# Kernel tuning notes

Measured on AMD Instinct MI355X. Metric: run time of the kernel, lower is better.

The kernel has to match this reference:

```python
import jax, jax.numpy as jnp
import numpy as np

N = 50000      # nodes
E = 800000     # edges
DIN, DH, DE, DOUT = 3, 32 and 3 or 3, 32, 1
DIN, DH, DE, DOUT = 3, 256, 32, 1
L = 5          # residual blocks
NEG_SLOPE = 0.2
EPS = 1e-16


def setup_inputs() -> dict:
    key = jax.random.key(0)
    ks = jax.random.split(key, 18)
    s = lambda d: 1.0 / np.sqrt(d)
    inp = {
        'x': jax.random.normal(ks[0], (N, DIN), jnp.float32),
        'edge_index': jax.random.randint(ks[1], (2, E), 0, N, jnp.int64),
        'edge_attr': jax.random.normal(ks[2], (E, DE), jnp.float32),
        # lin0 / lin1
        'W0': jax.random.normal(ks[3], (DIN, DH), jnp.float32) * s(DIN),
        'b0': jnp.zeros((DH,), jnp.float32),
        'W1': jax.random.normal(ks[4], (DH, DOUT), jnp.float32) * s(DH),
        'b1': jnp.zeros((DOUT,), jnp.float32),
        # per-block GAT params (stacked over L)
        'Wg': jax.random.normal(ks[5], (L, DH, DH), jnp.float32) * s(DH),
        'bg': jnp.zeros((L, DH), jnp.float32),
        'a_src': jax.random.normal(ks[6], (L, DH), jnp.float32) * s(DH),
        'a_dst': jax.random.normal(ks[7], (L, DH), jnp.float32) * s(DH),
        'We': jax.random.normal(ks[8], (L, DE, DH), jnp.float32) * s(DE),
        'a_e': jax.random.normal(ks[9], (L, DH), jnp.float32) * s(DH),
        # per-block mean-conv params
        'Ws': jax.random.normal(ks[10], (L, DH, DH), jnp.float32) * s(DH),
        'Wn': jax.random.normal(ks[11], (L, DH, DH), jnp.float32) * s(DH),
        'bm': jnp.zeros((L, DH), jnp.float32),
    }
    return inp


def _segment_softmax(logits, seg, n):
    m = jax.ops.segment_max(logits, seg, num_segments=n)          # [N]
    ex = jnp.exp(logits - m[seg])                                  # [E]
    den = jax.ops.segment_sum(ex, seg, num_segments=n)            # [N]
    return ex / (den[seg] + EPS)


def _block(x, src, dst, edge_attr, deg, Wg, bg, a_src, a_dst, We, a_e, Ws, Wn, bm):
    # GAT attention message passing (single head, edge-feature-aware logits)
    h = x @ Wg                                                     # [N,DH]
    logit = ((h * a_src).sum(-1)[src]
             + (h * a_dst).sum(-1)[dst]
             + ((edge_attr @ We) * a_e).sum(-1))                   # [E]
    logit = jax.nn.leaky_relu(logit, NEG_SLOPE)
    alpha = _segment_softmax(logit, dst, x.shape[0])               # [E]
    agg = jax.ops.segment_sum(alpha[:, None] * h[src], dst, num_segments=x.shape[0])
    h1 = jax.nn.relu(agg + bg)                                     # [N,DH]
    # mean-aggregation graph conv
    mean_nbr = jax.ops.segment_sum(h1[src], dst, num_segments=x.shape[0]) / deg[:, None]
    h2 = jax.nn.relu(h1 @ Ws + mean_nbr @ Wn + bm)
    return h2 + x                                                  # residual


def reference(x, edge_index, edge_attr, W0, b0, W1, b1, Wg, bg, a_src, a_dst, We, a_e, Ws, Wn, bm):
    src, dst = edge_index[0], edge_index[1]
    n = x.shape[0]
    deg = jnp.maximum(jax.ops.segment_sum(jnp.ones((src.shape[0],), x.dtype), dst, num_segments=n), 1.0)
    h = x @ W0 + b0
    for i in range(L):
        h = _block(h, src, dst, edge_attr, deg,
                   Wg[i], bg[i], a_src[i], a_dst[i], We[i], a_e[i], Ws[i], Wn[i], bm[i])
    return h @ W1 + b1
```

## Files before the change

kernel.cpp:

```cpp
#include <hip/hip_runtime.h>
#include <hip/hip_bf16.h>

#define DH 256
#define DE 32
#define NLAYERS 5
#define NEG_SLOPE 0.2f
#define EPSV 1e-16f
#define SEG 512

typedef __attribute__((ext_vector_type(8))) short bf16x8;
typedef __attribute__((ext_vector_type(4))) float f32x4;

__device__ inline float bf2f(unsigned short u) {
    unsigned x = ((unsigned)u) << 16;
    union { unsigned u; float f; } c; c.u = x; return c.f;
}
__device__ inline unsigned short f2bf(float f) {
    union { float f; unsigned u; } c; c.f = f;
    unsigned b = c.u;
    unsigned r = (b + 0x7FFF + ((b >> 16) & 1)) >> 16;
    return (unsigned short)r;
}

__global__ void k_count(const int* __restrict__ dst, int* __restrict__ cnt, int E) {
    int e = blockIdx.x * 256 + threadIdx.x;
    if (e < E) atomicAdd(&cnt[dst[e]], 1);
}

__global__ void k_part(const int* __restrict__ cnt, int* __restrict__ part, int n) {
    int b = blockIdx.x, t = threadIdx.x;
    int i = b * SEG + t;
    int v = (i < n) ? cnt[i] : 0;
    for (int d = 32; d; d >>= 1) v += __shfl_down(v, d);
    __shared__ int ws[8];
    int lane = t & 63, w = t >> 6;
    if (lane == 0) ws[w] = v;
    __syncthreads();
    if (t == 0) {
        int s = 0;
        #pragma unroll
        for (int k = 0; k < 8; ++k) s += ws[k];
        part[b] = s;
    }
}

__global__ void k_scanp(const int* __restrict__ part, int* __restrict__ base,
                        int* __restrict__ off, int nblk, int n, int total) {
    int t = threadIdx.x;
    int lane = t & 63, w = t >> 6;
    __shared__ int wsum[2];
    int v = (t < nblk) ? part[t] : 0;
    int incl = v;
    for (int d = 1; d < 64; d <<= 1) {
        int u = __shfl_up(incl, d);
        if (lane >= d) incl += u;
    }
    if (lane == 63) wsum[w] = incl;
    __syncthreads();
    int add = (w == 1) ? wsum[0] : 0;
    if (t < nblk) base[t] = incl - v + add;
    if (t == 0) off[n] = total;
}

__global__ void k_emit(const int* __restrict__ cnt, const int* __restrict__ base,
                       int* __restrict__ off, float* __restrict__ invd, int n) {
    int b = blockIdx.x, t = threadIdx.x;
    int i = b * SEG + t;
    int c = (i < n) ? cnt[i] : 0;
    int lane = t & 63, w = t >> 6;
    int incl = c;
    for (int d = 1; d < 64; d <<= 1) {
        int u = __shfl_up(incl, d);
        if (lane >= d) incl += u;
    }
    __shared__ int ws[8];
    if (lane == 63) ws[w] = incl;
    __syncthreads();
    int add = 0;
    for (int k = 0; k < w; ++k) add += ws[k];
    if (i < n) {
        off[i] = base[b] + add + incl - c;
        invd[i] = 1.0f / (float)max(c, 1);
    }
}

__global__ void k_fill(const int* __restrict__ src, const int* __restrict__ dst,
                       const int* __restrict__ off, int* __restrict__ cur,
                       int* __restrict__ csrc, int* __restrict__ pos, int E) {
    int e = blockIdx.x * 256 + threadIdx.x;
    if (e >= E) return;
    int d = dst[e];
    int p = off[d] + atomicAdd(&cur[d], 1);
    csrc[p] = src[e];
    pos[e] = p;
}

__global__ void k_we_ae(const float* __restrict__ We, const float* __restrict__ a_e,
                        float* __restrict__ out) {
    int t = threadIdx.x;
    if (t >= NLAYERS * DE) return;
    int l = t >> 5, d = t & 31;
    const float* w = We + ((size_t)l * DE + d) * DH;
    const float* ae = a_e + (size_t)l * DH;
    float s = 0.f;
    for (int j = 0; j < DH; ++j) s += w[j] * ae[j];
    out[t] = s;
}

__global__ void k_elogit(const float* __restrict__ ea, const float* __restrict__ we_ae,
                         const int* __restrict__ pos, float* __restrict__ elogp, int E) {
    __shared__ float w[NLAYERS * DE];
    if (threadIdx.x < NLAYERS * DE) w[threadIdx.x] = we_ae[threadIdx.x];
    __syncthreads();
    int e = blockIdx.x * 256 + threadIdx.x;
    if (e >= E) return;
    const float4* p = (const float4*)(ea + (size_t)e * DE);
    float r[NLAYERS] = {0, 0, 0, 0, 0};
    #pragma unroll
    for (int i = 0; i < DE / 4; ++i) {
        float4 x = p[i];
        #pragma unroll
        for (int l = 0; l < NLAYERS; ++l) {
            r[l] += x.x * w[l * DE + i * 4 + 0] + x.y * w[l * DE + i * 4 + 1] +
                    x.z * w[l * DE + i * 4 + 2] + x.w * w[l * DE + i * 4 + 3];
        }
    }
    int q = pos[e];
    #pragma unroll
    for (int l = 0; l < NLAYERS; ++l) elogp[(size_t)l * E + q] = r[l];
}

__global__ void k_wt(const float* __restrict__ Wg, const float* __restrict__ Ws,
                     const float* __restrict__ Wn, unsigned short* __restrict__ Wt) {
    __shared__ float tile[32][33];
    int z = blockIdx.z;
    const float* W = z < 5 ? Wg + (size_t)z * DH * DH
                   : (z < 10 ? Ws + (size_t)(z - 5) * DH * DH
                             : Wn + (size_t)(z - 10) * DH * DH);
    unsigned short* out = Wt + (size_t)z * DH * DH;
    int c0 = blockIdx.x * 32, r0 = blockIdx.y * 32;
    int tx = threadIdx.x, ty = threadIdx.y;
    for (int j = ty; j < 32; j += 8) tile[j][tx] = W[(size_t)(r0 + j) * DH + c0 + tx];
    __syncthreads();
    for (int j = ty; j < 32; j += 8)
        out[(size_t)(c0 + j) * DH + r0 + tx] = f2bf(tile[tx][j]);
}

__global__ void k_lin0(const float* __restrict__ x, const float* __restrict__ W0,
                       const float* __restrict__ b0, unsigned short* __restrict__ hb, int n) {
    int node = blockIdx.x;
    int c = threadIdx.x;
    if (node >= n) return;
    float x0 = x[(size_t)node * 3 + 0];
    float x1 = x[(size_t)node * 3 + 1];
    float x2 = x[(size_t)node * 3 + 2];
    float v = b0[c] + x0 * W0[c] + x1 * W0[DH + c] + x2 * W0[2 * DH + c];
    hb[(size_t)node * DH + c] = f2bf(v);
}

__global__ void k_dots(const unsigned short* __restrict__ hg, const float* __restrict__ asrc,
                       const float* __restrict__ adst, float* __restrict__ ssrc,
                       float* __restrict__ sdst, int n) {
    int wave = threadIdx.x >> 6, lane = threadIdx.x & 63;
    int row = blockIdx.x * 4 + wave;
    if (row >= n) return;
    ushort4 v = *(const ushort4*)(hg + (size_t)row * DH + lane * 4);
    float4 wa = *(const float4*)(asrc + lane * 4);
    float4 wb = *(const float4*)(adst + lane * 4);
    float f0 = bf2f(v.x), f1 = bf2f(v.y), f2 = bf2f(v.z), f3 = bf2f(v.w);
    float a = f0 * wa.x + f1 * wa.y + f2 * wa.z + f3 * wa.w;
    float b = f0 * wb.x + f1 * wb.y + f2 * wb.z + f3 * wb.w;
    for (int d = 32; d; d >>= 1) { a += __shfl_down(a, d); b += __shfl_down(b, d); }
    if (lane == 0) { ssrc[row] = a; sdst[row] = b; }
}

__global__ void k_attn(const int* __restrict__ off, const int* __restrict__ csrc,
                       const float* __restrict__ ssrc, const float* __restrict__ sdst,
                       const float* __restrict__ elogp, const unsigned short* __restrict__ hg,
                       const float* __restrict__ bias, unsigned short* __restrict__ h1, int n) {
    int wave = threadIdx.x >> 6, lane = threadIdx.x & 63;
    int node = blockIdx.x * 4 + wave;
    if (node >= n) return;
    int p0 = off[node], p1 = off[node + 1];
    int deg = p1 - p0;
    float sd = sdst[node];
    int c = lane * 4;
    float a0 = 0.f, a1 = 0.f, a2 = 0.f, a3 = 0.f;

    if (deg <= 256) {
        float ex0 = 0.f, ex1 = 0.f, ex2 = 0.f, ex3 = 0.f;
        int cs0 = 0, cs1 = 0, cs2 = 0, cs3 = 0;
        float m = -3.4e38f;
        {
            int p = p0 + lane;
            if (p < p1) { cs0 = csrc[p]; float r = ssrc[cs0] + sd + elogp[p];
                          r = r > 0.f ? r : NEG_SLOPE * r; ex0 = r; m = fmaxf(m, r); }
            p += 64;
            if (p < p1) { cs1 = csrc[p]; float r = ssrc[cs1] + sd + elogp[p];
                          r = r > 0.f ? r : NEG_SLOPE * r; ex1 = r; m = fmaxf(m, r); }
            p += 64;
            if (p < p1) { cs2 = csrc[p]; float r = ssrc[cs2] + sd + elogp[p];
                          r = r > 0.f ? r : NEG_SLOPE * r; ex2 = r; m = fmaxf(m, r); }
            p += 64;
            if (p < p1) { cs3 = csrc[p]; float r = ssrc[cs3] + sd + elogp[p];
                          r = r > 0.f ? r : NEG_SLOPE * r; ex3 = r; m = fmaxf(m, r); }
        }
        for (int d = 32; d; d >>= 1) m = fmaxf(m, __shfl_xor(m, d));
        float den = 0.f;
        {
            int p = p0 + lane;
            if (p < p1) { ex0 = expf(ex0 - m); den += ex0; }
            p += 64;
            if (p < p1) { ex1 = expf(ex1 - m); den += ex1; }
            p += 64;
            if (p < p1) { ex2 = expf(ex2 - m); den += ex2; }
            p += 64;
            if (p < p1) { ex3 = expf(ex3 - m); den += ex3; }
        }
        for (int d = 32; d; d >>= 1) den += __shfl_xor(den, d);
        float inv = 1.0f / (den + EPSV);

        #define EDGEA(u, WV, SV) { int q = p + (u) - p0; int jj = q >> 6; int sl = q & 63; \
            float ev = ex0; if (jj == 1) ev = ex1; else if (jj == 2) ev = ex2; else if (jj == 3) ev = ex3; \
            int cv = cs0; if (jj == 1) cv = cs1; else if (jj == 2) cv = cs2; else if (jj == 3) cv = cs3; \
            WV = __shfl(ev, sl) * inv; SV = __shfl(cv, sl); }

        int p = p0;
        for (; p + 4 <= p1; p += 4) {
            float w0, w1, w2, w3; int s0, s1, s2, s3;
            EDGEA(0, w0, s0) EDGEA(1, w1, s1) EDGEA(2, w2, s2) EDGEA(3, w3, s3)
            ushort4 v0 = *(const ushort4*)(hg + (size_t)s0 * DH + c);
            ushort4 v1 = *(const ushort4*)(hg + (size_t)s1 * DH + c);
            ushort4 v2 = *(const ushort4*)(hg + (size_t)s2 * DH + c);
            ushort4 v3 = *(const ushort4*)(hg + (size_t)s3 * DH + c);
            a0 += w0 * bf2f(v0.x) + w1 * bf2f(v1.x) + w2 * bf2f(v2.x) + w3 * bf2f(v3.x);
            a1 += w0 * bf2f(v0.y) + w1 * bf2f(v1.y) + w2 * bf2f(v2.y) + w3 * bf2f(v3.y);
            a2 += w0 * bf2f(v0.z) + w1 * bf2f(v1.z) + w2 * bf2f(v2.z) + w3 * bf2f(v3.z);
            a3 += w0 * bf2f(v0.w) + w1 * bf2f(v1.w) + w2 * bf2f(v2.w) + w3 * bf2f(v3.w);
        }
        for (; p < p1; ++p) {
            float w0; int s0;
            EDGEA(0, w0, s0)
            ushort4 v0 = *(const ushort4*)(hg + (size_t)s0 * DH + c);
            a0 += w0 * bf2f(v0.x); a1 += w0 * bf2f(v0.y);
            a2 += w0 * bf2f(v0.z); a3 += w0 * bf2f(v0.w);
        }
        #undef EDGEA
    } else {
        float m = -3.4e38f;
        for (int p = p0 + lane; p < p1; p += 64) {
            float r = ssrc[csrc[p]] + sd + elogp[p];
            r = r > 0.f ? r : NEG_SLOPE * r;
            m = fmaxf(m, r);
        }
        for (int d = 32; d; d >>= 1) m = fmaxf(m, __shfl_xor(m, d));
        float den = 0.f;
        for (int p = p0 + lane; p < p1; p += 64) {
            float r = ssrc[csrc[p]] + sd + elogp[p];
            r = r > 0.f ? r : NEG_SLOPE * r;
            den += expf(r - m);
        }
        for (int d = 32; d; d >>= 1) den += __shfl_xor(den, d);
        float inv = 1.0f / (den + EPSV);
        for (int p = p0; p < p1; ++p) {
            int sn = csrc[p];
            float r = ssrc[sn] + sd + elogp[p];
            r = r > 0.f ? r : NEG_SLOPE * r;
            float a = expf(r - m) * inv;
            ushort4 v = *(const ushort4*)(hg + (size_t)sn * DH + c);
            a0 += a * bf2f(v.x); a1 += a * bf2f(v.y);
            a2 += a * bf2f(v.z); a3 += a * bf2f(v.w);
        }
    }

    float4 bb = *(const float4*)(bias + c);
    ushort4 o;
    o.x = f2bf(fmaxf(a0 + bb.x, 0.f));
    o.y = f2bf(fmaxf(a1 + bb.y, 0.f));
    o.z = f2bf(fmaxf(a2 + bb.z, 0.f));
    o.w = f2bf(fmaxf(a3 + bb.w, 0.f));
    *(ushort4*)(h1 + (size_t)node * DH + c) = o;
}

__global__ void k_mean(const int* __restrict__ off, const int* __restrict__ csrc,
                       const unsigned short* __restrict__ h1, const float* __restrict__ inv_deg,
                       unsigned short* __restrict__ mean, int n) {
    int wave = threadIdx.x >> 6, lane = threadIdx.x & 63;
    int node = blockIdx.x * 4 + wave;
    if (node >= n) return;
    int p0 = off[node], p1 = off[node + 1];
    int c = lane * 4;
    float a0 = 0.f, a1 = 0.f, a2 = 0.f, a3 = 0.f;
    int p = p0;
    for (; p + 4 <= p1; p += 4) {
        int s0 = csrc[p], s1 = csrc[p + 1], s2 = csrc[p + 2], s3 = csrc[p + 3];
        ushort4 v0 = *(const ushort4*)(h1 + (size_t)s0 * DH + c);
        ushort4 v1 = *(const ushort4*)(h1 + (size_t)s1 * DH + c);
        ushort4 v2 = *(const ushort4*)(h1 + (size_t)s2 * DH + c);
        ushort4 v3 = *(const ushort4*)(h1 + (size_t)s3 * DH + c);
        a0 += bf2f(v0.x) + bf2f(v1.x) + bf2f(v2.x) + bf2f(v3.x);
        a1 += bf2f(v0.y) + bf2f(v1.y) + bf2f(v2.y) + bf2f(v3.y);
        a2 += bf2f(v0.z) + bf2f(v1.z) + bf2f(v2.z) + bf2f(v3.z);
        a3 += bf2f(v0.w) + bf2f(v1.w) + bf2f(v2.w) + bf2f(v3.w);
    }
    for (; p < p1; ++p) {
        ushort4 v = *(const ushort4*)(h1 + (size_t)csrc[p] * DH + c);
        a0 += bf2f(v.x); a1 += bf2f(v.y); a2 += bf2f(v.z); a3 += bf2f(v.w);
    }
    float inv = inv_deg[node];
    ushort4 o;
    o.x = f2bf(a0 * inv); o.y = f2bf(a1 * inv);
    o.z = f2bf(a2 * inv); o.w = f2bf(a3 * inv);
    *(ushort4*)(mean + (size_t)node * DH + c) = o;
}

__global__ void k_out(const unsigned short* __restrict__ h, const float* __restrict__ W1,
                      const float* __restrict__ b1, float* __restrict__ out, int n) {
    int wave = threadIdx.x >> 6, lane = threadIdx.x & 63;
    int row = blockIdx.x * 4 + wave;
    if (row >= n) return;
    ushort4 v = *(const ushort4*)(h + (size_t)row * DH + lane * 4);
    float4 w1 = *(const float4*)(W1 + lane * 4);
    float s = bf2f(v.x) * w1.x + bf2f(v.y) * w1.y + bf2f(v.z) * w1.z + bf2f(v.w) * w1.w;
    for (int d = 32; d; d >>= 1) s += __shfl_down(s, d);
    if (lane == 0) out[row] = s + b1[0];
}

template <int TWO, int EPI>
__global__ __launch_bounds__(256) void k_gemm_mfma(
    const unsigned short* __restrict__ A, const unsigned short* __restrict__ Bt,
    const unsigned short* __restrict__ A2, const unsigned short* __restrict__ B2t,
    const float* __restrict__ bias, const unsigned short* __restrict__ resid,
    unsigned short* __restrict__ Cb, int M) {
    const int t = threadIdx.x;
    const int wid = t >> 6, lane = t & 63;
    const int wr = wid >> 1, wc = wid & 1;
    const int bm = blockIdx.x * 128 + wr * 64;
    const int bn = blockIdx.y * 128 + wc * 64;
    const int lrow = lane & 15;
    const int kgrp = (lane >> 4) * 8;

    f32x4 acc[4][4] = {};

    #pragma unroll
    for (int pass = 0; pass <= TWO; ++pass) {
        const unsigned short* Ap = pass ? A2 : A;
        const unsigned short* Bp = pass ? B2t : Bt;
        #pragma unroll 2
        for (int k0 = 0; k0 < DH; k0 += 32) {
            bf16x8 a[4], b[4];
            #pragma unroll
            for (int m = 0; m < 4; ++m)
                a[m] = *(const bf16x8*)(Ap + (size_t)(bm + m * 16 + lrow) * DH + k0 + kgrp);
            #pragma unroll
            for (int n = 0; n < 4; ++n)
                b[n] = *(const bf16x8*)(Bp + (size_t)(bn + n * 16 + lrow) * DH + k0 + kgrp);
            #pragma unroll
            for (int m = 0; m < 4; ++m)
                #pragma unroll
                for (int n = 0; n < 4; ++n)
                    acc[m][n] = __builtin_amdgcn_mfma_f32_16x16x32_bf16(a[m], b[n], acc[m][n], 0, 0, 0);
        }
    }

    const int crow0 = (lane >> 4) * 4;
    #pragma unroll
    for (int m = 0; m < 4; ++m) {
        #pragma unroll
        for (int r = 0; r < 4; ++r) {
            int row = bm + m * 16 + crow0 + r;
            if (row >= M) continue;
            #pragma unroll
            for (int n = 0; n < 4; ++n) {
                int col = bn + n * 16 + lrow;
                size_t idx = (size_t)row * DH + col;
                float v = acc[m][n][r];
                if (EPI) {
                    v += bias[col];
                    v = fmaxf(v, 0.f);
                    v += bf2f(resid[idx]);
                }
                Cb[idx] = f2bf(v);
            }
        }
    }
}

extern "C" void kernel_launch(void* const* d_in, const int* in_sizes, int n_in,
                              void* d_out, int out_size, void* d_ws, size_t ws_size,
                              hipStream_t stream) {
    const float* x    = (const float*)d_in[0];
    const int*   ei   = (const int*)d_in[1];
    const float* ea   = (const float*)d_in[2];
    const float* W0   = (const float*)d_in[3];
    const float* b0   = (const float*)d_in[4];
    const float* W1   = (const float*)d_in[5];
    const float* b1   = (const float*)d_in[6];
    const float* Wg   = (const float*)d_in[7];
    const float* bg   = (const float*)d_in[8];
    const float* a_src= (const float*)d_in[9];
    const float* a_dst= (const float*)d_in[10];
    const float* We   = (const float*)d_in[11];
    const float* a_e  = (const float*)d_in[12];
    const float* Ws   = (const float*)d_in[13];
    const float* Wn   = (const float*)d_in[14];
    const float* bm   = (const float*)d_in[15];
    float* out = (float*)d_out;

    const int N = in_sizes[0] / 3;
    const int E = in_sizes[1] / 2;
    const int Mpad = (N + 127) & ~127;
    const int* srcI = ei;
    const int* dstI = ei + E;

    char* p = (char*)d_ws;
    auto alloc = [&](size_t bytes) {
        void* r = (void*)p;
        p += (bytes + 255) & ~(size_t)255;
        return r;
    };
    size_t NBh = (size_t)Mpad * DH * sizeof(unsigned short);
    unsigned short* Hb0  = (unsigned short*)alloc(NBh);
    unsigned short* Hb1  = (unsigned short*)alloc(NBh);
    unsigned short* hgbf = (unsigned short*)alloc(NBh);
    unsigned short* h1bf = (unsigned short*)alloc(NBh);
    unsigned short* Wt   = (unsigned short*)alloc((size_t)15 * DH * DH * sizeof(unsigned short));
    float* elogp = (float*)alloc((size_t)NLAYERS * E * sizeof(float));
    int*   csrc  = (int*)alloc((size_t)E * sizeof(int));
    int*   pos   = (int*)alloc((size_t)E * sizeof(int));
    int*   off   = (int*)alloc((size_t)(N + 1) * sizeof(int));
    int*   cnt   = (int*)alloc((size_t)N * sizeof(int));
    int*   cur   = (int*)alloc((size_t)N * sizeof(int));
    float* invd  = (float*)alloc((size_t)N * sizeof(float));
    float* ssrc  = (float*)alloc((size_t)N * sizeof(float));
    float* sdst  = (float*)alloc((size_t)N * sizeof(float));
    float* weae  = (float*)alloc((size_t)NLAYERS * DE * sizeof(float));
    const int NBLK = (N + SEG - 1) / SEG;
    int* part = (int*)alloc((size_t)NBLK * sizeof(int));
    int* base = (int*)alloc((size_t)NBLK * sizeof(int));

    const int EB = (E + 255) / 256;
    const int NB4 = (N + 3) / 4;
    const int MB = Mpad / 128;

    hipMemsetAsync(cnt, 0, (size_t)N * sizeof(int), stream);
    hipMemsetAsync(cur, 0, (size_t)N * sizeof(int), stream);
    k_count<<<EB, 256, 0, stream>>>(dstI, cnt, E);
    k_part<<<NBLK, SEG, 0, stream>>>(cnt, part, N);
    k_scanp<<<1, 128, 0, stream>>>(part, base, off, NBLK, N, E);
    k_emit<<<NBLK, SEG, 0, stream>>>(cnt, base, off, invd, N);
    k_fill<<<EB, 256, 0, stream>>>(srcI, dstI, off, cur, csrc, pos, E);

    k_we_ae<<<1, 256, 0, stream>>>(We, a_e, weae);
    k_elogit<<<EB, 256, 0, stream>>>(ea, weae, pos, elogp, E);
    k_wt<<<dim3(8, 8, 15), dim3(32, 8), 0, stream>>>(Wg, Ws, Wn, Wt);

    k_lin0<<<N, DH, 0, stream>>>(x, W0, b0, Hb0, N);

    unsigned short* Hcur = Hb0;
    unsigned short* Hnxt = Hb1;
    for (int l = 0; l < NLAYERS; ++l) {
        const unsigned short* Wgt = Wt + (size_t)l * DH * DH;
        const unsigned short* Wst = Wt + (size_t)(5 + l) * DH * DH;
        const unsigned short* Wnt = Wt + (size_t)(10 + l) * DH * DH;
        unsigned short* meanbf = hgbf;

        k_gemm_mfma<0, 0><<<dim3(MB, 2), 256, 0, stream>>>(
            Hcur, Wgt, nullptr, nullptr, nullptr, nullptr, hgbf, N);
        k_dots<<<NB4, 256, 0, stream>>>(hgbf, a_src + (size_t)l * DH, a_dst + (size_t)l * DH,
                                        ssrc, sdst, N);
        k_attn<<<NB4, 256, 0, stream>>>(off, csrc, ssrc, sdst, elogp + (size_t)l * E,
                                        hgbf, bg + (size_t)l * DH, h1bf, N);
        k_mean<<<NB4, 256, 0, stream>>>(off, csrc, h1bf, invd, meanbf, N);
        k_gemm_mfma<1, 1><<<dim3(MB, 2), 256, 0, stream>>>(
            h1bf, Wst, meanbf, Wnt, bm + (size_t)l * DH, Hcur, Hnxt, N);

        unsigned short* tmp = Hcur; Hcur = Hnxt; Hnxt = tmp;
    }

    k_out<<<NB4, 256, 0, stream>>>(Hcur, W1, b1, out, N);
}
```

Baseline: 1.528 ms.

## Fuse attention dot products into GEMM epilogue, unroll gathers, write edge logits in CSR order

New measurement: 1.560 ms. 1.02x slower.

```diff
diff --git a/kernel.cpp b/kernel.cpp
--- a/kernel.cpp
+++ b/kernel.cpp
@@ -86,13 +86,13 @@
 
 __global__ void k_fill(const int* __restrict__ src, const int* __restrict__ dst,
                        const int* __restrict__ off, int* __restrict__ cur,
-                       int* __restrict__ csrc, int* __restrict__ pos, int E) {
+                       int* __restrict__ csrc, int* __restrict__ ceid, int E) {
     int e = blockIdx.x * 256 + threadIdx.x;
     if (e >= E) return;
     int d = dst[e];
     int p = off[d] + atomicAdd(&cur[d], 1);
     csrc[p] = src[e];
-    pos[e] = p;
+    ceid[p] = e;
 }
 
 __global__ void k_we_ae(const float* __restrict__ We, const float* __restrict__ a_e,
@@ -108,26 +108,26 @@
 }
 
 __global__ void k_elogit(const float* __restrict__ ea, const float* __restrict__ we_ae,
-                         const int* __restrict__ pos, float* __restrict__ elogp, int E) {
+                         const int* __restrict__ ceid, float* __restrict__ elogp, int E) {
     __shared__ float w[NLAYERS * DE];
     if (threadIdx.x < NLAYERS * DE) w[threadIdx.x] = we_ae[threadIdx.x];
     __syncthreads();
-    int e = blockIdx.x * 256 + threadIdx.x;
-    if (e >= E) return;
-    const float4* p = (const float4*)(ea + (size_t)e * DE);
+    int p = blockIdx.x * 256 + threadIdx.x;
+    if (p >= E) return;
+    int e = ceid[p];
+    const float4* q = (const float4*)(ea + (size_t)e * DE);
     float r[NLAYERS] = {0, 0, 0, 0, 0};
     #pragma unroll
     for (int i = 0; i < DE / 4; ++i) {
-        float4 x = p[i];
+        float4 x = q[i];
         #pragma unroll
         for (int l = 0; l < NLAYERS; ++l) {
             r[l] += x.x * w[l * DE + i * 4 + 0] + x.y * w[l * DE + i * 4 + 1] +
                     x.z * w[l * DE + i * 4 + 2] + x.w * w[l * DE + i * 4 + 3];
         }
     }
-    int q = pos[e];
     #pragma unroll
-    for (int l = 0; l < NLAYERS; ++l) elogp[(size_t)l * E + q] = r[l];
+    for (int l = 0; l < NLAYERS; ++l) elogp[(size_t)l * E + p] = r[l];
 }
 
 __global__ void k_wt(const float* __restrict__ Wg, const float* __restrict__ Ws,
@@ -156,22 +156,6 @@
     float x2 = x[(size_t)node * 3 + 2];
     float v = b0[c] + x0 * W0[c] + x1 * W0[DH + c] + x2 * W0[2 * DH + c];
     hb[(size_t)node * DH + c] = f2bf(v);
-}
-
-__global__ void k_dots(const unsigned short* __restrict__ hg, const float* __restrict__ asrc,
-                       const float* __restrict__ adst, float* __restrict__ ssrc,
-                       float* __restrict__ sdst, int n) {
-    int wave = threadIdx.x >> 6, lane = threadIdx.x & 63;
-    int row = blockIdx.x * 4 + wave;
-    if (row >= n) return;
-    ushort4 v = *(const ushort4*)(hg + (size_t)row * DH + lane * 4);
-    float4 wa = *(const float4*)(asrc + lane * 4);
-    float4 wb = *(const float4*)(adst + lane * 4);
-    float f0 = bf2f(v.x), f1 = bf2f(v.y), f2 = bf2f(v.z), f3 = bf2f(v.w);
-    float a = f0 * wa.x + f1 * wa.y + f2 * wa.z + f3 * wa.w;
-    float b = f0 * wb.x + f1 * wb.y + f2 * wb.z + f3 * wb.w;
-    for (int d = 32; d; d >>= 1) { a += __shfl_down(a, d); b += __shfl_down(b, d); }
-    if (lane == 0) { ssrc[row] = a; sdst[row] = b; }
 }
 
 __global__ void k_attn(const int* __restrict__ off, const int* __restrict__ csrc,
@@ -226,17 +210,27 @@
             WV = __shfl(ev, sl) * inv; SV = __shfl(cv, sl); }
 
         int p = p0;
-        for (; p + 4 <= p1; p += 4) {
-            float w0, w1, w2, w3; int s0, s1, s2, s3;
+        for (; p + 8 <= p1; p += 8) {
+            float w0, w1, w2, w3, w4, w5, w6, w7;
+            int s0, s1, s2, s3, s4, s5, s6, s7;
             EDGEA(0, w0, s0) EDGEA(1, w1, s1) EDGEA(2, w2, s2) EDGEA(3, w3, s3)
+            EDGEA(4, w4, s4) EDGEA(5, w5, s5) EDGEA(6, w6, s6) EDGEA(7, w7, s7)
             ushort4 v0 = *(const ushort4*)(hg + (size_t)s0 * DH + c);
             ushort4 v1 = *(const ushort4*)(hg + (size_t)s1 * DH + c);
             ushort4 v2 = *(const ushort4*)(hg + (size_t)s2 * DH + c);
             ushort4 v3 = *(const ushort4*)(hg + (size_t)s3 * DH + c);
-            a0 += w0 * bf2f(v0.x) + w1 * bf2f(v1.x) + w2 * bf2f(v2.x) + w3 * bf2f(v3.x);
-            a1 += w0 * bf2f(v0.y) + w1 * bf2f(v1.y) + w2 * bf2f(v2.y) + w3 * bf2f(v3.y);
-            a2 += w0 * bf2f(v0.z) + w1 * bf2f(v1.z) + w2 * bf2f(v2.z) + w3 * bf2f(v3.z);
-            a3 += w0 * bf2f(v0.w) + w1 * bf2f(v1.w) + w2 * bf2f(v2.w) + w3 * bf2f(v3.w);
+            ushort4 v4 = *(const ushort4*)(hg + (size_t)s4 * DH + c);
+            ushort4 v5 = *(const ushort4*)(hg + (size_t)s5 * DH + c);
+            ushort4 v6 = *(const ushort4*)(hg + (size_t)s6 * DH + c);
+            ushort4 v7 = *(const ushort4*)(hg + (size_t)s7 * DH + c);
+            a0 += w0 * bf2f(v0.x) + w1 * bf2f(v1.x) + w2 * bf2f(v2.x) + w3 * bf2f(v3.x)
+                + w4 * bf2f(v4.x) + w5 * bf2f(v5.x) + w6 * bf2f(v6.x) + w7 * bf2f(v7.x);
+            a1 += w0 * bf2f(v0.y) + w1 * bf2f(v1.y) + w2 * bf2f(v2.y) + w3 * bf2f(v3.y)
+                + w4 * bf2f(v4.y) + w5 * bf2f(v5.y) + w6 * bf2f(v6.y) + w7 * bf2f(v7.y);
+            a2 += w0 * bf2f(v0.z) + w1 * bf2f(v1.z) + w2 * bf2f(v2.z) + w3 * bf2f(v3.z)
+                + w4 * bf2f(v4.z) + w5 * bf2f(v5.z) + w6 * bf2f(v6.z) + w7 * bf2f(v7.z);
+            a3 += w0 * bf2f(v0.w) + w1 * bf2f(v1.w) + w2 * bf2f(v2.w) + w3 * bf2f(v3.w)
+                + w4 * bf2f(v4.w) + w5 * bf2f(v5.w) + w6 * bf2f(v6.w) + w7 * bf2f(v7.w);
         }
         for (; p < p1; ++p) {
             float w0; int s0;
@@ -292,16 +286,25 @@
     int c = lane * 4;
     float a0 = 0.f, a1 = 0.f, a2 = 0.f, a3 = 0.f;
     int p = p0;
-    for (; p + 4 <= p1; p += 4) {
-        int s0 = csrc[p], s1 = csrc[p + 1], s2 = csrc[p + 2], s3 = csrc[p + 3];
+    for (; p + 8 <= p1; p += 8) {
+        int s0 = csrc[p],     s1 = csrc[p + 1], s2 = csrc[p + 2], s3 = csrc[p + 3];
+        int s4 = csrc[p + 4], s5 = csrc[p + 5], s6 = csrc[p + 6], s7 = csrc[p + 7];
         ushort4 v0 = *(const ushort4*)(h1 + (size_t)s0 * DH + c);
         ushort4 v1 = *(const ushort4*)(h1 + (size_t)s1 * DH + c);
         ushort4 v2 = *(const ushort4*)(h1 + (size_t)s2 * DH + c);
         ushort4 v3 = *(const ushort4*)(h1 + (size_t)s3 * DH + c);
-        a0 += bf2f(v0.x) + bf2f(v1.x) + bf2f(v2.x) + bf2f(v3.x);
-        a1 += bf2f(v0.y) + bf2f(v1.y) + bf2f(v2.y) + bf2f(v3.y);
-        a2 += bf2f(v0.z) + bf2f(v1.z) + bf2f(v2.z) + bf2f(v3.z);
-        a3 += bf2f(v0.w) + bf2f(v1.w) + bf2f(v2.w) + bf2f(v3.w);
+        ushort4 v4 = *(const ushort4*)(h1 + (size_t)s4 * DH + c);
+        ushort4 v5 = *(const ushort4*)(h1 + (size_t)s5 * DH + c);
+        ushort4 v6 = *(const ushort4*)(h1 + (size_t)s6 * DH + c);
+        ushort4 v7 = *(const ushort4*)(h1 + (size_t)s7 * DH + c);
+        a0 += bf2f(v0.x) + bf2f(v1.x) + bf2f(v2.x) + bf2f(v3.x)
+            + bf2f(v4.x) + bf2f(v5.x) + bf2f(v6.x) + bf2f(v7.x);
+        a1 += bf2f(v0.y) + bf2f(v1.y) + bf2f(v2.y) + bf2f(v3.y)
+            + bf2f(v4.y) + bf2f(v5.y) + bf2f(v6.y) + bf2f(v7.y);
+        a2 += bf2f(v0.z) + bf2f(v1.z) + bf2f(v2.z) + bf2f(v3.z)
+            + bf2f(v4.z) + bf2f(v5.z) + bf2f(v6.z) + bf2f(v7.z);
+        a3 += bf2f(v0.w) + bf2f(v1.w) + bf2f(v2.w) + bf2f(v3.w)
+            + bf2f(v4.w) + bf2f(v5.w) + bf2f(v6.w) + bf2f(v7.w);
     }
     for (; p < p1; ++p) {
         ushort4 v = *(const ushort4*)(h1 + (size_t)csrc[p] * DH + c);
@@ -326,12 +329,14 @@
     if (lane == 0) out[row] = s + b1[0];
 }
 
-template <int TWO, int EPI>
+template <int TWO, int EPI, int DOTS>
 __global__ __launch_bounds__(256) void k_gemm_mfma(
     const unsigned short* __restrict__ A, const unsigned short* __restrict__ Bt,
     const unsigned short* __restrict__ A2, const unsigned short* __restrict__ B2t,
     const float* __restrict__ bias, const unsigned short* __restrict__ resid,
-    unsigned short* __restrict__ Cb, int M) {
+    unsigned short* __restrict__ Cb, int M,
+    const float* __restrict__ asrc, const float* __restrict__ adst,
+    float* __restrict__ ssrc, float* __restrict__ sdst) {
     const int t = threadIdx.x;
     const int wid = t >> 6, lane = t & 63;
     const int wr = wid >> 1, wc = wid & 1;
@@ -363,6 +368,15 @@
         }
     }
 
+    float wa[4], wb[4];
+    if (DOTS) {
+        #pragma unroll
+        for (int n = 0; n < 4; ++n) {
+            wa[n] = asrc[bn + n * 16 + lrow];
+            wb[n] = adst[bn + n * 16 + lrow];
+        }
+    }
+
     const int crow0 = (lane >> 4) * 4;
     #pragma unroll
     for (int m = 0; m < 4; ++m) {
@@ -370,6 +384,7 @@
         for (int r = 0; r < 4; ++r) {
             int row = bm + m * 16 + crow0 + r;
             if (row >= M) continue;
+            float ds = 0.f, dd = 0.f;
             #pragma unroll
             for (int n = 0; n < 4; ++n) {
                 int col = bn + n * 16 + lrow;
@@ -381,6 +396,18 @@
                     v += bf2f(resid[idx]);
                 }
                 Cb[idx] = f2bf(v);
+                if (DOTS) { ds += v * wa[n]; dd += v * wb[n]; }
+            }
+            if (DOTS) {
+                #pragma unroll
+                for (int d = 1; d < 16; d <<= 1) {
+                    ds += __shfl_xor(ds, d);
+                    dd += __shfl_xor(dd, d);
+                }
+                if (lrow == 0) {
+                    atomicAdd(&ssrc[row], ds);
+                    atomicAdd(&sdst[row], dd);
+                }
             }
         }
     }
@@ -427,13 +454,14 @@
     unsigned short* Wt   = (unsigned short*)alloc((size_t)15 * DH * DH * sizeof(unsigned short));
     float* elogp = (float*)alloc((size_t)NLAYERS * E * sizeof(float));
     int*   csrc  = (int*)alloc((size_t)E * sizeof(int));
-    int*   pos   = (int*)alloc((size_t)E * sizeof(int));
+    int*   ceid  = (int*)alloc((size_t)E * sizeof(int));
     int*   off   = (int*)alloc((size_t)(N + 1) * sizeof(int));
     int*   cnt   = (int*)alloc((size_t)N * sizeof(int));
     int*   cur   = (int*)alloc((size_t)N * sizeof(int));
     float* invd  = (float*)alloc((size_t)N * sizeof(float));
-    float* ssrc  = (float*)alloc((size_t)N * sizeof(float));
-    float* sdst  = (float*)alloc((size_t)N * sizeof(float));
+    float* sdots = (float*)alloc((size_t)2 * N * sizeof(float));
+    float* ssrc  = sdots;
+    float* sdst  = sdots + N;
     float* weae  = (float*)alloc((size_t)NLAYERS * DE * sizeof(float));
     const int NBLK = (N + SEG - 1) / SEG;
     int* part = (int*)alloc((size_t)NBLK * sizeof(int));
@@ -449,10 +477,10 @@
     k_part<<<NBLK, SEG, 0, stream>>>(cnt, part, N);
     k_scanp<<<1, 128, 0, stream>>>(part, base, off, NBLK, N, E);
     k_emit<<<NBLK, SEG, 0, stream>>>(cnt, base, off, invd, N);
-    k_fill<<<EB, 256, 0, stream>>>(srcI, dstI, off, cur, csrc, pos, E);
+    k_fill<<<EB, 256, 0, stream>>>(srcI, dstI, off, cur, csrc, ceid, E);
 
     k_we_ae<<<1, 256, 0, stream>>>(We, a_e, weae);
-    k_elogit<<<EB, 256, 0, stream>>>(ea, weae, pos, elogp, E);
+    k_elogit<<<EB, 256, 0, stream>>>(ea, weae, ceid, elogp, E);
     k_wt<<<dim3(8, 8, 15), dim3(32, 8), 0, stream>>>(Wg, Ws, Wn, Wt);
 
     k_lin0<<<N, DH, 0, stream>>>(x, W0, b0, Hb0, N);
@@ -465,15 +493,16 @@
         const unsigned short* Wnt = Wt + (size_t)(10 + l) * DH * DH;
         unsigned short* meanbf = hgbf;
 
-        k_gemm_mfma<0, 0><<<dim3(MB, 2), 256, 0, stream>>>(
-            Hcur, Wgt, nullptr, nullptr, nullptr, nullptr, hgbf, N);
-        k_dots<<<NB4, 256, 0, stream>>>(hgbf, a_src + (size_t)l * DH, a_dst + (size_t)l * DH,
-                                        ssrc, sdst, N);
+        hipMemsetAsync(sdots, 0, (size_t)2 * N * sizeof(float), stream);
+        k_gemm_mfma<0, 0, 1><<<dim3(MB, 2), 256, 0, stream>>>(
+            Hcur, Wgt, nullptr, nullptr, nullptr, nullptr, hgbf, N,
+            a_src + (size_t)l * DH, a_dst + (size_t)l * DH, ssrc, sdst);
         k_attn<<<NB4, 256, 0, stream>>>(off, csrc, ssrc, sdst, elogp + (size_t)l * E,
                                         hgbf, bg + (size_t)l * DH, h1bf, N);
         k_mean<<<NB4, 256, 0, stream>>>(off, csrc, h1bf, invd, meanbf, N);
-        k_gemm_mfma<1, 1><<<dim3(MB, 2), 256, 0, stream>>>(
-            h1bf, Wst, meanbf, Wnt, bm + (size_t)l * DH, Hcur, Hnxt, N);
+        k_gemm_mfma<1, 1, 0><<<dim3(MB, 2), 256, 0, stream>>>(
+            h1bf, Wst, meanbf, Wnt, bm + (size_t)l * DH, Hcur, Hnxt, N,
+            nullptr, nullptr, nullptr, nullptr);
 
         unsigned short* tmp = Hcur; Hcur = Hnxt; Hnxt = tmp;
     }
```
